# Kernel optimization log

Measured on AMD Instinct MI355X. Metric: run time of the kernel, lower is better.

## Reference

```python
import jax, jax.numpy as jnp
import numpy as np

D_IN = 2048
D_OUT = 2048
NUM_HEADS = 16
HEAD_DIM = D_OUT // NUM_HEADS
CONTEXT_LENGTH = 4096
THETA_BASE = 10000.0


def _rope_tables(seq_len):
    half = HEAD_DIM // 2
    inv_freq = 1.0 / (THETA_BASE ** (jnp.arange(half, dtype=jnp.float32) / half))
    positions = jnp.arange(seq_len, dtype=jnp.float32)
    angles = positions[:, None] * inv_freq[None, :]          # [S, half]
    angles = jnp.concatenate([angles, angles], axis=-1)      # [S, HEAD_DIM]
    return jnp.cos(angles), jnp.sin(angles)


def _apply_rope(x, cos, sin):
    # x: [B, H, S, D]
    half = x.shape[-1] // 2
    x1, x2 = x[..., :half], x[..., half:]
    rotated = jnp.concatenate([-x2, x1], axis=-1)
    return x * cos[None, None, :, :] + rotated * sin[None, None, :, :]


def setup_inputs() -> dict:
    key = jax.random.key(0)
    ks = jax.random.split(key, 5)
    x = jax.random.normal(ks[0], (1, 4096, D_IN), dtype=jnp.float32)
    scale_in = 1.0 / np.sqrt(D_IN)
    scale_out = 1.0 / np.sqrt(D_OUT)
    w_q = jax.random.normal(ks[1], (D_OUT, D_IN), dtype=jnp.float32) * scale_in
    w_k = jax.random.normal(ks[2], (D_OUT, D_IN), dtype=jnp.float32) * scale_in
    w_v = jax.random.normal(ks[3], (D_OUT, D_IN), dtype=jnp.float32) * scale_in
    w_o = jax.random.normal(ks[4], (D_IN, D_OUT), dtype=jnp.float32) * scale_out
    return {"x": x, "w_q": w_q, "w_k": w_k, "w_v": w_v, "w_o": w_o}


def reference(x, w_q, w_k, w_v, w_o):
    b, s, _ = x.shape
    cos, sin = _rope_tables(s)

    def split_heads(t):  # [B,S,D_OUT] -> [B,H,S,HEAD_DIM]
        return t.reshape(b, s, NUM_HEADS, HEAD_DIM).transpose(0, 2, 1, 3)

    q = split_heads(jnp.einsum('bsd,od->bso', x, w_q))
    k = split_heads(jnp.einsum('bsd,od->bso', x, w_k))
    v = split_heads(jnp.einsum('bsd,od->bso', x, w_v))

    q = _apply_rope(q, cos, sin)
    k = _apply_rope(k, cos, sin)

    scores = jnp.einsum('bhqd,bhkd->bhqk', q, k) / jnp.sqrt(jnp.float32(HEAD_DIM))
    causal = jnp.tril(jnp.ones((s, s), dtype=bool))
    scores = jnp.where(causal[None, None, :, :], scores, -jnp.inf)
    attn = jax.nn.softmax(scores, axis=-1)

    ctx = jnp.einsum('bhqk,bhkd->bhqd', attn, v)  # [B,H,S,HEAD_DIM]
    ctx = ctx.transpose(0, 2, 1, 3).reshape(b, s, D_OUT)
    return jnp.einsum('bso,do->bsd', ctx, w_o)
```

## Files before the change

kernel.cpp:

```cpp
#include <hip/hip_runtime.h>
#include <hip/hip_bf16.h>
#include <stdint.h>

#define SEQ 4096
#define DM 2048
#define NH 16
#define HD 128

typedef __attribute__((ext_vector_type(4)))  float f32x4;
typedef __attribute__((ext_vector_type(16))) float f32x16;
typedef __attribute__((ext_vector_type(8)))  short bf16x8;
typedef __attribute__((ext_vector_type(4)))  float float4_t;
typedef __attribute__((ext_vector_type(4)))  short s16x4;
typedef __attribute__((ext_vector_type(2)))  int   i32x2;
typedef __attribute__((ext_vector_type(2)))  unsigned u32x2;

__device__ __forceinline__ short f2bf(float f) {
  union { float f; unsigned u; } c; c.f = f;
  unsigned u = c.u;
  u += 0x7FFFu + ((u >> 16) & 1u);
  return (short)(u >> 16);
}

__device__ __forceinline__ int cvtpk(float lo, float hi) {
  int r;
  asm("v_cvt_pk_bf16_f32 %0, %1, %2" : "=v"(r) : "v"(lo), "v"(hi));
  return r;
}

__device__ __forceinline__ float exp2r(float x) {
  return __builtin_amdgcn_exp2f(x);
}

__device__ __forceinline__ void async16(const void* g, void* l) {
  __builtin_amdgcn_global_load_lds((const __attribute__((address_space(1))) void*)g,
                                   (__attribute__((address_space(3))) void*)l, 16, 0, 0);
}

__global__ __launch_bounds__(256) void rope_tables_kernel(float2* __restrict__ tab) {
  int idx = blockIdx.x * 256 + threadIdx.x;
  int s = idx >> 6, j = idx & 63;
  float invf = expf(-(float)j * (9.210340371976184f / 64.0f));
  float ang = (float)s * invf;
  tab[idx] = make_float2(cosf(ang), sinf(ang));
}

__global__ __launch_bounds__(256) void f32_to_bf16_kernel(const float* __restrict__ in,
                                                          short* __restrict__ out, int n4) {
  int stride = gridDim.x * 256;
  for (int i = blockIdx.x * 256 + threadIdx.x; i < n4; i += stride) {
    float4_t v = ((const float4_t*)in)[i];
    s16x4 r;
    #pragma unroll
    for (int u = 0; u < 4; u++) r[u] = f2bf(v[u]);
    ((s16x4*)out)[i] = r;
  }
}

__global__ __launch_bounds__(256) void w3_to_bf16_kernel(
    const float* __restrict__ wq, const float* __restrict__ wk,
    const float* __restrict__ wv, short* __restrict__ out) {
  const int n4w = DM * DM / 4;
  int stride = gridDim.x * 256;
  for (int i = blockIdx.x * 256 + threadIdx.x; i < 3 * n4w; i += stride) {
    int j = i >> 20;
    int loc = i & (n4w - 1);
    const float* src = (j == 0) ? wq : (j == 1) ? wk : wv;
    float4_t v = ((const float4_t*)src)[loc];
    s16x4 r;
    #pragma unroll
    for (int u = 0; u < 4; u++) r[u] = f2bf(v[u]);
    ((s16x4*)out)[i] = r;
  }
}

__global__ __launch_bounds__(512) void gemm_qkv_kernel(
    const short* __restrict__ A, const short* __restrict__ B,
    short* __restrict__ Qout, short* __restrict__ Kout, short* __restrict__ VTout,
    const float2* __restrict__ tab, int region) {
  constexpr int NN = DM, K = DM, MM = SEQ;
  __shared__ __align__(16) char LB[147456];
  const int t = threadIdx.x, lane = t & 63, w = t >> 6;
  const int wm = w >> 1, wn = w & 1;
  const size_t Mbase = (size_t)blockIdx.x * 256;
  const int ry  = (region < 0) ? (blockIdx.y >> 4) : region;
  const int nyl = (region < 0) ? (blockIdx.y & 15) : blockIdx.y;
  const size_t Bbase = (size_t)blockIdx.y * 128;
  const size_t Nbase = (size_t)nyl * 128;
  const int nt = K / 64;

  auto stageA = [&](int kt, int half) {
    const int buf = kt % 3, k0 = kt * 64;
    #pragma unroll
    for (int it = 0; it < 2; it++) {
      const int ob = half * 16384 + it * 8192 + w * 1024;
      const int o = ob + lane * 16;
      const int row = o >> 7;
      const int col = (o & 127) ^ ((row & 7) << 4);
      async16((const char*)A + ((Mbase + row) * (size_t)K + k0) * 2 + col,
              LB + buf * 32768 + ob);
    }
  };
  auto stageB = [&](int kt) {
    const int buf = kt % 3, k0 = kt * 64;
    #pragma unroll
    for (int it = 0; it < 2; it++) {
      const int ob = it * 8192 + w * 1024;
      const int o = ob + lane * 16;
      const int row = o >> 7;
      const int col = (o & 127) ^ ((row & 7) << 4);
      async16((const char*)B + ((Bbase + row) * (size_t)K + k0) * 2 + col,
              LB + 98304 + buf * 16384 + ob);
    }
  };

  f32x4 acc[4][4] = {};

  stageA(0, 0); stageA(0, 1); stageB(0);
  stageA(1, 0); stageA(1, 1); stageB(1);
  asm volatile("s_waitcnt vmcnt(6)" ::: "memory");
  __builtin_amdgcn_s_barrier();

  for (int kt = 0; kt < nt; kt++) {
    const char* AsB = LB + (kt % 3) * 32768;
    const char* BsB = LB + 98304 + (kt % 3) * 16384;
    const bool pre = (kt + 2 < nt);
    bf16x8 a[2][4], b[2][2];

    #pragma unroll
    for (int ks = 0; ks < 2; ks++)
      #pragma unroll
      for (int m = 0; m < 4; m++) {
        int row = wm * 64 + m * 16 + (lane & 15);
        a[ks][m] = *(const bf16x8*)(AsB + row * 128
                    + ((ks * 64 + (lane >> 4) * 16) ^ ((row & 7) << 4)));
      }
    #pragma unroll
    for (int ks = 0; ks < 2; ks++)
      #pragma unroll
      for (int n = 0; n < 2; n++) {
        int row = n * 32 + wn * 16 + (lane & 15);
        b[ks][n] = *(const bf16x8*)(BsB + row * 128
                    + ((ks * 64 + (lane >> 4) * 16) ^ ((row & 7) << 4)));
      }
    if (pre) { stageA(kt + 2, 0); stageA(kt + 2, 1); }
    __builtin_amdgcn_s_barrier();
    asm volatile("s_waitcnt lgkmcnt(0)" ::: "memory");
    __builtin_amdgcn_sched_barrier(0);
    __builtin_amdgcn_s_setprio(1);
    #pragma unroll
    for (int ks = 0; ks < 2; ks++)
      #pragma unroll
      for (int m = 0; m < 4; m++)
        #pragma unroll
        for (int n = 0; n < 2; n++)
          acc[m][n] = __builtin_amdgcn_mfma_f32_16x16x32_bf16(
              a[ks][m], b[ks][n], acc[m][n], 0, 0, 0);
    __builtin_amdgcn_s_setprio(0);
    __builtin_amdgcn_s_barrier();

    #pragma unroll
    for (int ks = 0; ks < 2; ks++)
      #pragma unroll
      for (int n = 0; n < 2; n++) {
        int row = (n + 2) * 32 + wn * 16 + (lane & 15);
        b[ks][n] = *(const bf16x8*)(BsB + row * 128
                    + ((ks * 64 + (lane >> 4) * 16) ^ ((row & 7) << 4)));
      }
    if (pre) stageB(kt + 2);
    if (pre) asm volatile("s_waitcnt vmcnt(6)" ::: "memory");
    else     asm volatile("s_waitcnt vmcnt(0)" ::: "memory");
    __builtin_amdgcn_s_barrier();
    asm volatile("s_waitcnt lgkmcnt(0)" ::: "memory");
    __builtin_amdgcn_sched_barrier(0);
    __builtin_amdgcn_s_setprio(1);
    #pragma unroll
    for (int ks = 0; ks < 2; ks++)
      #pragma unroll
      for (int m = 0; m < 4; m++)
        #pragma unroll
        for (int n = 0; n < 2; n++)
          acc[m][n + 2] = __builtin_amdgcn_mfma_f32_16x16x32_bf16(
              a[ks][m], b[ks][n], acc[m][n + 2], 0, 0, 0);
    __builtin_amdgcn_s_setprio(0);
    __builtin_amdgcn_s_barrier();
  }

  if (ry < 2) {
    const float SC = (ry == 0) ? 0.12751746f : 1.0f;
    short* C = (ry == 0) ? Qout : Kout;
    #pragma unroll
    for (int m = 0; m < 4; m++)
      #pragma unroll
      for (int n = 0; n < 2; n++)
        #pragma unroll
        for (int j = 0; j < 4; j++) {
          int row = (int)Mbase + wm * 64 + m * 16 + (lane >> 4) * 4 + j;
          int dj = n * 32 + wn * 16 + (lane & 15);
          float2 cs = tab[row * 64 + dj];
          float cc = cs.x * SC, ss = cs.y * SC;
          float r1 = acc[m][n][j], r2 = acc[m][n + 2][j];
          C[(size_t)row * NN + Nbase + dj]      = f2bf(r1 * cc - r2 * ss);
          C[(size_t)row * NN + Nbase + dj + 64] = f2bf(r2 * cc + r1 * ss);
        }
  } else {
    #pragma unroll
    for (int m = 0; m < 4; m++)
      #pragma unroll
      for (int n = 0; n < 4; n++)
        #pragma unroll
        for (int j = 0; j < 4; j++) {
          size_t row = Mbase + wm * 64 + m * 16 + (lane >> 4) * 4 + j;
          size_t col = Nbase + n * 32 + wn * 16 + (lane & 15);
          VTout[col * (size_t)MM + row] = f2bf(acc[m][n][j]);
        }
  }
}

__global__ __launch_bounds__(512) void gemm_out_kernel(
    const short* __restrict__ A, const short* __restrict__ B,
    float* __restrict__ Cp) {
  constexpr int NN = DM, K = DM;
  __shared__ __align__(16) char LB[147456];
  const int t = threadIdx.x, lane = t & 63, w = t >> 6;
  const int wm = w >> 1, wn = w & 1;
  const size_t Mbase = (size_t)blockIdx.x * 256;
  const size_t Nbase = (size_t)blockIdx.y * 128;
  const int nt = K / 64;

  auto stageA = [&](int kt, int half) {
    const int buf = kt % 3, k0 = kt * 64;
    #pragma unroll
    for (int it = 0; it < 2; it++) {
      const int ob = half * 16384 + it * 8192 + w * 1024;
      const int o = ob + lane * 16;
      const int row = o >> 7;
      const int col = (o & 127) ^ ((row & 7) << 4);
      async16((const char*)A + ((Mbase + row) * (size_t)K + k0) * 2 + col,
              LB + buf * 32768 + ob);
    }
  };
  auto stageB = [&](int kt) {
    const int buf = kt % 3, k0 = kt * 64;
    #pragma unroll
    for (int it = 0; it < 2; it++) {
      const int ob = it * 8192 + w * 1024;
      const int o = ob + lane * 16;
      const int row = o >> 7;
      const int col = (o & 127) ^ ((row & 7) << 4);
      async16((const char*)B + ((Nbase + row) * (size_t)K + k0) * 2 + col,
              LB + 98304 + buf * 16384 + ob);
    }
  };

  f32x4 acc[4][4] = {};

  stageA(0, 0); stageA(0, 1); stageB(0);
  stageA(1, 0); stageA(1, 1); stageB(1);
  asm volatile("s_waitcnt vmcnt(6)" ::: "memory");
  __builtin_amdgcn_s_barrier();

  for (int kt = 0; kt < nt; kt++) {
    const char* AsB = LB + (kt % 3) * 32768;
    const char* BsB = LB + 98304 + (kt % 3) * 16384;
    const bool pre = (kt + 2 < nt);
    bf16x8 a[2][4], b[2][2];

    #pragma unroll
    for (int ks = 0; ks < 2; ks++)
      #pragma unroll
      for (int m = 0; m < 4; m++) {
        int row = wm * 64 + m * 16 + (lane & 15);
        a[ks][m] = *(const bf16x8*)(AsB + row * 128
                    + ((ks * 64 + (lane >> 4) * 16) ^ ((row & 7) << 4)));
      }
    #pragma unroll
    for (int ks = 0; ks < 2; ks++)
      #pragma unroll
      for (int n = 0; n < 2; n++) {
        int row = n * 32 + wn * 16 + (lane & 15);
        b[ks][n] = *(const bf16x8*)(BsB + row * 128
                    + ((ks * 64 + (lane >> 4) * 16) ^ ((row & 7) << 4)));
      }
    if (pre) { stageA(kt + 2, 0); stageA(kt + 2, 1); }
    __builtin_amdgcn_s_barrier();
    asm volatile("s_waitcnt lgkmcnt(0)" ::: "memory");
    __builtin_amdgcn_sched_barrier(0);
    __builtin_amdgcn_s_setprio(1);
    #pragma unroll
    for (int ks = 0; ks < 2; ks++)
      #pragma unroll
      for (int m = 0; m < 4; m++)
        #pragma unroll
        for (int n = 0; n < 2; n++)
          acc[m][n] = __builtin_amdgcn_mfma_f32_16x16x32_bf16(
              a[ks][m], b[ks][n], acc[m][n], 0, 0, 0);
    __builtin_amdgcn_s_setprio(0);
    __builtin_amdgcn_s_barrier();

    #pragma unroll
    for (int ks = 0; ks < 2; ks++)
      #pragma unroll
      for (int n = 0; n < 2; n++) {
        int row = (n + 2) * 32 + wn * 16 + (lane & 15);
        b[ks][n] = *(const bf16x8*)(BsB + row * 128
                    + ((ks * 64 + (lane >> 4) * 16) ^ ((row & 7) << 4)));
      }
    if (pre) stageB(kt + 2);
    if (pre) asm volatile("s_waitcnt vmcnt(6)" ::: "memory");
    else     asm volatile("s_waitcnt vmcnt(0)" ::: "memory");
    __builtin_amdgcn_s_barrier();
    asm volatile("s_waitcnt lgkmcnt(0)" ::: "memory");
    __builtin_amdgcn_sched_barrier(0);
    __builtin_amdgcn_s_setprio(1);
    #pragma unroll
    for (int ks = 0; ks < 2; ks++)
      #pragma unroll
      for (int m = 0; m < 4; m++)
        #pragma unroll
        for (int n = 0; n < 2; n++)
          acc[m][n + 2] = __builtin_amdgcn_mfma_f32_16x16x32_bf16(
              a[ks][m], b[ks][n], acc[m][n + 2], 0, 0, 0);
    __builtin_amdgcn_s_setprio(0);
    __builtin_amdgcn_s_barrier();
  }

  #pragma unroll
  for (int m = 0; m < 4; m++)
    #pragma unroll
    for (int n = 0; n < 4; n++)
      #pragma unroll
      for (int j = 0; j < 4; j++) {
        size_t row = Mbase + wm * 64 + m * 16 + (lane >> 4) * 4 + j;
        size_t col = Nbase + n * 32 + wn * 16 + (lane & 15);
        Cp[row * NN + col] = acc[m][n][j];
      }
}

__global__ __launch_bounds__(512) void flash_attn9_kernel(
    const short* __restrict__ Q, const short* __restrict__ K,
    const short* __restrict__ VT, short* __restrict__ O) {
  __shared__ __align__(16) char LB[65536];
  const int t = threadIdx.x, lane = t & 63, w = t >> 6;
  const int hi = lane >> 5, c31 = lane & 31;
  const int s = w & 3, v = w >> 2;
  const int id = blockIdx.x;
  const int h  = (id & 7) * 2 + ((id >> 3) & 1);
  const int pr = (id >> 4) & 15;
  const int qt = (id < 256) ? pr : (31 - pr);

  auto stage = [&](int kt, int buf) {
    #pragma unroll
    for (int it = 0; it < 2; it++) {
      const int ob = it * 8192 + w * 1024;
      const int o  = ob + lane * 16;
      const int row = o >> 8;
      const int xs = (o & 255) ^ ((row & 15) << 4);
      { const size_t src = ((size_t)(kt * 64 + row) * DM + h * HD) * 2 + xs;
        async16((const char*)K + src, LB + buf * 16384 + ob); }
      { const int d = 2 * row + (xs >> 7);
        const size_t src = ((size_t)(h * HD + d) * SEQ + (size_t)kt * 64) * 2
                         + (size_t)(xs & 127);
        async16((const char*)VT + src, LB + 32768 + buf * 16384 + ob); }
    }
  };

  const int q0 = qt * 128;
  const int nt = 2 * (qt + 1);
  const int qrow = q0 + s * 32 + c31;

  stage(0, 0);

  bf16x8 qf[8];
  #pragma unroll
  for (int ss = 0; ss < 8; ss++)
    qf[ss] = *(const bf16x8*)(Q + (size_t)qrow * DM + h * HD + ss * 16 + hi * 8);

  f32x16 oacc[4] = {};
  float m = -3.0e38f, l = 0.f;

  __syncthreads();

  for (int kt = 0; kt < nt; kt++) {
    const int buf = kt & 1;
    if (kt + 1 < nt) stage(kt + 1, buf ^ 1);

    if (kt * 64 + v * 32 <= q0 + s * 32 + 31) {
      const char* KsB = LB + buf * 16384;
      const char* VsB = LB + 32768 + buf * 16384;

      f32x16 sacc = {};
      __builtin_amdgcn_s_setprio(1);
      #pragma unroll
      for (int ss = 0; ss < 8; ss++) {
        int row = v * 32 + c31;
        bf16x8 kf = *(const bf16x8*)(KsB + row * 256
                                     + ((ss * 32 + hi * 16) ^ ((row & 15) << 4)));
        sacc = __builtin_amdgcn_mfma_f32_32x32x16_bf16(kf, qf[ss], sacc, 0, 0, 0);
      }
      __builtin_amdgcn_s_setprio(0);

      float t0[8];
      #pragma unroll
      for (int r = 0; r < 8; r++) t0[r] = fmaxf(sacc[r], sacc[r + 8]);
      #pragma unroll
      for (int d = 4; d > 0; d >>= 1)
        #pragma unroll
        for (int r = 0; r < 4; r++) if (r < d) t0[r] = fmaxf(t0[r], t0[r + d]);
      float mx = t0[0];
      i32x2 mm = __builtin_amdgcn_permlane32_swap(__float_as_int(mx), __float_as_int(mx),
                                                  false, false);
      mx = fmaxf(__int_as_float(mm.x), __int_as_float(mm.y));

      if (__any(mx > m + 11.5416f)) {
        float mn = fmaxf(m, mx);
        float al = exp2r(m - mn);
        m = mn; l *= al;
        #pragma unroll
        for (int g = 0; g < 4; g++)
          #pragma unroll
          for (int r = 0; r < 16; r++) oacc[g][r] *= al;
      }

      const int rel = qrow - kt * 64 - v * 32;
      const bool maskT = (kt * 64 + v * 32 + 31) > (q0 + s * 32);
      #pragma unroll
      for (int r = 0; r < 16; r++) {
        float e = exp2r(sacc[r] - m);
        if (maskT) {
          int kl = (r & 3) + 8 * (r >> 2) + 4 * hi;
          e = (kl > rel) ? 0.f : e;
        }
        sacc[r] = e;
      }

      float s0[8];
      #pragma unroll
      for (int r = 0; r < 8; r++) s0[r] = sacc[r] + sacc[r + 8];
      #pragma unroll
      for (int d = 4; d > 0; d >>= 1)
        #pragma unroll
        for (int r = 0; r < 4; r++) if (r < d) s0[r] = s0[r] + s0[r + d];
      l += s0[0];

      bf16x8 pa[2];
      #pragma unroll
      for (int sg = 0; sg < 2; sg++) {
        int q0a = cvtpk(sacc[8 * sg + 0], sacc[8 * sg + 1]);
        int q1a = cvtpk(sacc[8 * sg + 2], sacc[8 * sg + 3]);
        int q0b = cvtpk(sacc[8 * sg + 4], sacc[8 * sg + 5]);
        int q1b = cvtpk(sacc[8 * sg + 6], sacc[8 * sg + 7]);
        i32x2 r0 = __builtin_amdgcn_permlane32_swap(q0a, q0b, false, false);
        i32x2 r1 = __builtin_amdgcn_permlane32_swap(q1a, q1b, false, false);
        union { int d[4]; bf16x8 vv; } u;
        u.d[0] = r0.x; u.d[1] = r1.x; u.d[2] = r0.y; u.d[3] = r1.y;
        pa[sg] = u.vv;
      }

      __builtin_amdgcn_s_setprio(1);
      #pragma unroll
      for (int ks = 0; ks < 2; ks++)
        #pragma unroll
        for (int g = 0; g < 4; g++) {
          int d = g * 32 + c31;
          int row = d >> 1;
          int x = (d & 1) * 128 + v * 64 + ks * 32 + hi * 16;
          bf16x8 vf = *(const bf16x8*)(VsB + row * 256 + (x ^ ((row & 15) << 4)));
          oacc[g] = __builtin_amdgcn_mfma_f32_32x32x16_bf16(vf, pa[ks], oacc[g], 0, 0, 0);
        }
      __builtin_amdgcn_s_setprio(0);
    }
    __syncthreads();
  }

  i32x2 lr = __builtin_amdgcn_permlane32_swap(__float_as_int(l), __float_as_int(l),
                                              false, false);
  l = __int_as_float(lr.x) + __int_as_float(lr.y);

  #pragma unroll
  for (int round = 0; round < 2; round++) {
    const int reg = s & 1;
    const bool active = (s >> 1) == round;
    if (active && v == 1) {
      float* Op = (float*)(LB + reg * 16384);
      #pragma unroll
      for (int g = 0; g < 4; g++)
        #pragma unroll
        for (int rr = 0; rr < 16; rr++) {
          int d = g * 32 + (rr & 3) + 8 * (rr >> 2) + 4 * hi;
          Op[d * 32 + c31] = oacc[g][rr];
        }
      if (hi == 0) {
        float* mm2 = (float*)(LB + 32768 + reg * 256) + c31 * 2;
        mm2[0] = m; mm2[1] = l;
      }
    }
    __syncthreads();
    if (active && v == 0) {
      const float* mm2 = (const float*)(LB + 32768 + reg * 256) + c31 * 2;
      float lB = mm2[1];
      float mB = (lB > 0.f) ? mm2[0] : -3.0e38f;
      float ms = fmaxf(m, mB);
      float aA = exp2r(m - ms), aB = exp2r(mB - ms);
      float linv = 1.0f / (l * aA + lB * aB);
      float sA = aA * linv, sB = aB * linv;
      const float* Op = (const float*)(LB + reg * 16384);
      #pragma unroll
      for (int g = 0; g < 4; g++)
        #pragma unroll
        for (int tt = 0; tt < 4; tt++) {
          float o[4];
          #pragma unroll
          for (int e = 0; e < 4; e++) {
            int d = g * 32 + e + 8 * tt + 4 * hi;
            o[e] = oacc[g][4 * tt + e] * sA + Op[d * 32 + c31] * sB;
          }
          u32x2 pk;
          pk.x = (unsigned)cvtpk(o[0], o[1]);
          pk.y = (unsigned)cvtpk(o[2], o[3]);
          *(u32x2*)(O + (size_t)qrow * DM + h * HD + g * 32 + tt * 8 + hi * 4) = pk;
        }
    }
    __syncthreads();
  }
}

extern "C" void kernel_launch(void* const* d_in, const int* in_sizes, int n_in,
                              void* d_out, int out_size, void* d_ws, size_t ws_size,
                              hipStream_t stream) {
  const float* x  = (const float*)d_in[0];
  const float* wq = (const float*)d_in[1];
  const float* wk = (const float*)d_in[2];
  const float* wv = (const float*)d_in[3];
  const float* wo = (const float*)d_in[4];
  float* out = (float*)d_out;

  const size_t SQDMs = (size_t)SEQ * DM;
  short* Qb   = (short*)d_ws;
  short* Kb   = Qb + SQDMs;
  short* VTb  = Kb + SQDMs;
  short* Cb   = VTb + SQDMs;
  short* xbf  = Cb + SQDMs;
  short* wbuf = xbf + SQDMs;

  const bool fused = ws_size >= (size_t)107 * 1024 * 1024;
  float2* tab = (float2*)(wbuf + (fused ? (size_t)3 * DM * DM : (size_t)DM * DM));

  rope_tables_kernel<<<SEQ * 64 / 256, 256, 0, stream>>>(tab);
  f32_to_bf16_kernel<<<2048, 256, 0, stream>>>(x, xbf, (int)(SQDMs / 4));

  if (fused) {
    w3_to_bf16_kernel<<<2048, 256, 0, stream>>>(wq, wk, wv, wbuf);
    gemm_qkv_kernel<<<dim3(SEQ / 256, 48), 512, 0, stream>>>(
        xbf, wbuf, Qb, Kb, VTb, tab, -1);
  } else {
    f32_to_bf16_kernel<<<2048, 256, 0, stream>>>(wq, wbuf, DM * DM / 4);
    gemm_qkv_kernel<<<dim3(SEQ / 256, 16), 512, 0, stream>>>(
        xbf, wbuf, Qb, Kb, VTb, tab, 0);
    f32_to_bf16_kernel<<<2048, 256, 0, stream>>>(wk, wbuf, DM * DM / 4);
    gemm_qkv_kernel<<<dim3(SEQ / 256, 16), 512, 0, stream>>>(
        xbf, wbuf, Qb, Kb, VTb, tab, 1);
    f32_to_bf16_kernel<<<2048, 256, 0, stream>>>(wv, wbuf, DM * DM / 4);
    gemm_qkv_kernel<<<dim3(SEQ / 256, 16), 512, 0, stream>>>(
        xbf, wbuf, Qb, Kb, VTb, tab, 2);
  }

  flash_attn9_kernel<<<512, 512, 0, stream>>>(Qb, Kb, VTb, Cb);

  f32_to_bf16_kernel<<<2048, 256, 0, stream>>>(wo, wbuf, DM * DM / 4);
  gemm_out_kernel<<<dim3(SEQ / 256, DM / 128), 512, 0, stream>>>(Cb, wbuf, out);
}
```

Before: 275.2 us.

## Collapse per-iteration GEMM barriers into one end-of-iteration barrier

In both projection GEMM kernels the main loop used four workgroup barriers per k-tile plus split prefetch stages. Now all A and B prefetches for tile kt+2 are issued together, the second B fragment loads go into a separate register set, and one combined vmcnt/lgkmcnt wait and barrier sits at the end of each iteration. This cuts barrier stalls and lets LDS reads and MFMAs overlap more freely. The cost is extra registers for the second B fragment set and reliance on the triple-buffered LDS ring to keep the reduced synchronisation safe.

New measurement: 271.9 us (median of 2 runs). Within noise of the previous version (-1.2%).

```diff
diff --git a/kernel.cpp b/kernel.cpp
--- a/kernel.cpp
+++ b/kernel.cpp
@@ -125,7 +125,7 @@
     const char* AsB = LB + (kt % 3) * 32768;
     const char* BsB = LB + 98304 + (kt % 3) * 16384;
     const bool pre = (kt + 2 < nt);
-    bf16x8 a[2][4], b[2][2];
+    bf16x8 a[2][4], b[2][2], b2[2][2];
 
     #pragma unroll
     for (int ks = 0; ks < 2; ks++)
@@ -143,10 +143,8 @@
         b[ks][n] = *(const bf16x8*)(BsB + row * 128
                     + ((ks * 64 + (lane >> 4) * 16) ^ ((row & 7) << 4)));
       }
-    if (pre) { stageA(kt + 2, 0); stageA(kt + 2, 1); }
-    __builtin_amdgcn_s_barrier();
-    asm volatile("s_waitcnt lgkmcnt(0)" ::: "memory");
-    __builtin_amdgcn_sched_barrier(0);
+    if (pre) { stageA(kt + 2, 0); stageA(kt + 2, 1); stageB(kt + 2); }
+
     __builtin_amdgcn_s_setprio(1);
     #pragma unroll
     for (int ks = 0; ks < 2; ks++)
@@ -157,22 +155,15 @@
           acc[m][n] = __builtin_amdgcn_mfma_f32_16x16x32_bf16(
               a[ks][m], b[ks][n], acc[m][n], 0, 0, 0);
     __builtin_amdgcn_s_setprio(0);
-    __builtin_amdgcn_s_barrier();
 
     #pragma unroll
     for (int ks = 0; ks < 2; ks++)
       #pragma unroll
       for (int n = 0; n < 2; n++) {
         int row = (n + 2) * 32 + wn * 16 + (lane & 15);
-        b[ks][n] = *(const bf16x8*)(BsB + row * 128
-                    + ((ks * 64 + (lane >> 4) * 16) ^ ((row & 7) << 4)));
-      }
-    if (pre) stageB(kt + 2);
-    if (pre) asm volatile("s_waitcnt vmcnt(6)" ::: "memory");
-    else     asm volatile("s_waitcnt vmcnt(0)" ::: "memory");
-    __builtin_amdgcn_s_barrier();
-    asm volatile("s_waitcnt lgkmcnt(0)" ::: "memory");
-    __builtin_amdgcn_sched_barrier(0);
+        b2[ks][n] = *(const bf16x8*)(BsB + row * 128
+                     + ((ks * 64 + (lane >> 4) * 16) ^ ((row & 7) << 4)));
+      }
     __builtin_amdgcn_s_setprio(1);
     #pragma unroll
     for (int ks = 0; ks < 2; ks++)
@@ -181,9 +172,15 @@
         #pragma unroll
         for (int n = 0; n < 2; n++)
           acc[m][n + 2] = __builtin_amdgcn_mfma_f32_16x16x32_bf16(
-              a[ks][m], b[ks][n], acc[m][n + 2], 0, 0, 0);
+              a[ks][m], b2[ks][n], acc[m][n + 2], 0, 0, 0);
     __builtin_amdgcn_s_setprio(0);
-    __builtin_amdgcn_s_barrier();
+
+    if (kt + 1 < nt) {
+      if (pre) asm volatile("s_waitcnt vmcnt(6) lgkmcnt(0)" ::: "memory");
+      else     asm volatile("s_waitcnt vmcnt(0) lgkmcnt(0)" ::: "memory");
+      __builtin_amdgcn_sched_barrier(0);
+      __builtin_amdgcn_s_barrier();
+    }
   }
 
   if (ry < 2) {
@@ -264,7 +261,7 @@
     const char* AsB = LB + (kt % 3) * 32768;
     const char* BsB = LB + 98304 + (kt % 3) * 16384;
     const bool pre = (kt + 2 < nt);
-    bf16x8 a[2][4], b[2][2];
+    bf16x8 a[2][4], b[2][2], b2[2][2];
 
     #pragma unroll
     for (int ks = 0; ks < 2; ks++)
@@ -282,10 +279,8 @@
         b[ks][n] = *(const bf16x8*)(BsB + row * 128
                     + ((ks * 64 + (lane >> 4) * 16) ^ ((row & 7) << 4)));
       }
-    if (pre) { stageA(kt + 2, 0); stageA(kt + 2, 1); }
-    __builtin_amdgcn_s_barrier();
-    asm volatile("s_waitcnt lgkmcnt(0)" ::: "memory");
-    __builtin_amdgcn_sched_barrier(0);
+    if (pre) { stageA(kt + 2, 0); stageA(kt + 2, 1); stageB(kt + 2); }
+
     __builtin_amdgcn_s_setprio(1);
     #pragma unroll
     for (int ks = 0; ks < 2; ks++)
@@ -296,22 +291,15 @@
           acc[m][n] = __builtin_amdgcn_mfma_f32_16x16x32_bf16(
               a[ks][m], b[ks][n], acc[m][n], 0, 0, 0);
     __builtin_amdgcn_s_setprio(0);
-    __builtin_amdgcn_s_barrier();
 
     #pragma unroll
     for (int ks = 0; ks < 2; ks++)
       #pragma unroll
       for (int n = 0; n < 2; n++) {
         int row = (n + 2) * 32 + wn * 16 + (lane & 15);
-        b[ks][n] = *(const bf16x8*)(BsB + row * 128
-                    + ((ks * 64 + (lane >> 4) * 16) ^ ((row & 7) << 4)));
-      }
-    if (pre) stageB(kt + 2);
-    if (pre) asm volatile("s_waitcnt vmcnt(6)" ::: "memory");
-    else     asm volatile("s_waitcnt vmcnt(0)" ::: "memory");
-    __builtin_amdgcn_s_barrier();
-    asm volatile("s_waitcnt lgkmcnt(0)" ::: "memory");
-    __builtin_amdgcn_sched_barrier(0);
+        b2[ks][n] = *(const bf16x8*)(BsB + row * 128
+                     + ((ks * 64 + (lane >> 4) * 16) ^ ((row & 7) << 4)));
+      }
     __builtin_amdgcn_s_setprio(1);
     #pragma unroll
     for (int ks = 0; ks < 2; ks++)
@@ -320,9 +308,15 @@
         #pragma unroll
         for (int n = 0; n < 2; n++)
           acc[m][n + 2] = __builtin_amdgcn_mfma_f32_16x16x32_bf16(
-              a[ks][m], b[ks][n], acc[m][n + 2], 0, 0, 0);
+              a[ks][m], b2[ks][n], acc[m][n + 2], 0, 0, 0);
     __builtin_amdgcn_s_setprio(0);
-    __builtin_amdgcn_s_barrier();
+
+    if (kt + 1 < nt) {
+      if (pre) asm volatile("s_waitcnt vmcnt(6) lgkmcnt(0)" ::: "memory");
+      else     asm volatile("s_waitcnt vmcnt(0) lgkmcnt(0)" ::: "memory");
+      __builtin_amdgcn_sched_barrier(0);
+      __builtin_amdgcn_s_barrier();
+    }
   }
 
   #pragma unroll
```
